# Kernel optimization log

Hardware: AMD Instinct MI355X
Metric: run time of the kernel (lower is better)

The kernel has to match this reference:

```python
import jax, jax.numpy as jnp
import numpy as np

EPS = 1e-5  # torch InstanceNorm2d default eps


def conv1x1(x, w, b):
    # x: [B,C,H,W], w: [O,C], b: [O]
    return jnp.einsum('bchw,oc->bohw', x, w) + b[None, :, None, None]


def conv3x3(x, w, b):
    y = jax.lax.conv_general_dilated(x, w, (1, 1), 'SAME',
                                     dimension_numbers=('NCHW', 'OIHW', 'NCHW'))
    return y + b[None, :, None, None]


def inorm(x):
    # InstanceNorm2d, affine=False, biased variance
    m = jnp.mean(x, axis=(2, 3), keepdims=True)
    v = jnp.var(x, axis=(2, 3), keepdims=True)
    return (x - m) * jax.lax.rsqrt(v + EPS)


def self_attn(x, wq, bq, wk, bk, wv, bv, gamma):
    B, C, H, W = x.shape
    N = H * W
    q = conv1x1(x, wq, bq).reshape(B, -1, N)   # [B,C/8,N]
    k = conv1x1(x, wk, bk).reshape(B, -1, N)   # [B,C/8,N]
    A = jax.nn.softmax(jnp.einsum('bdn,bdm->bnm', q, k), axis=-1)  # [B,N,N]
    v = conv1x1(x, wv, bv).reshape(B, C, N)    # [B,C,N]
    out = jnp.einsum('bcm,bnm->bcn', v, A).reshape(B, C, H, W)
    return gamma * out + x


def setup_inputs() -> dict:
    key = jax.random.key(0)
    B, C, H, W = 2, 256, 64, 64
    C8 = C // 8
    ks = iter(jax.random.split(key, 40))

    def n(shape, scale=0.05):
        return jax.random.normal(next(ks), shape, dtype=jnp.float32) * scale

    inp = {
        'x': jax.random.normal(next(ks), (B, C, H, W), dtype=jnp.float32),
        'y': jax.random.normal(next(ks), (B, C, H, W), dtype=jnp.float32),
    }
    for p in ('sa1', 'sa2', 'top'):
        inp[p + '_wq'] = n((C8, C)); inp[p + '_bq'] = n((C8,))
        inp[p + '_wk'] = n((C8, C)); inp[p + '_bk'] = n((C8,))
        inp[p + '_wv'] = n((C, C));  inp[p + '_bv'] = n((C,))
        inp[p + '_gamma'] = n((1,), 0.1)
    inp['conv1_w'] = n((C, C, 3, 3)); inp['conv1_b'] = n((C,))
    inp['conv2_w'] = n((C, C, 3, 3)); inp['conv2_b'] = n((C,))
    return inp


def reference(x, y,
              sa1_wq, sa1_bq, sa1_wk, sa1_bk, sa1_wv, sa1_bv, sa1_gamma,
              sa2_wq, sa2_bq, sa2_wk, sa2_bk, sa2_wv, sa2_bv, sa2_gamma,
              top_wq, top_bq, top_wk, top_bk, top_wv, top_bv, top_gamma,
              conv1_w, conv1_b, conv2_w, conv2_b):
    out_1 = inorm(self_attn(x, sa1_wq, sa1_bq, sa1_wk, sa1_bk, sa1_wv, sa1_bv, sa1_gamma))
    out_2 = inorm(out_1 + conv3x3(out_1, conv1_w, conv1_b))
    out_3 = inorm(self_attn(y, sa2_wq, sa2_bq, sa2_wk, sa2_bk, sa2_wv, sa2_bv, sa2_gamma))

    B, C, H, W = out_2.shape
    N = H * W
    q = conv1x1(out_2, top_wq, top_bq).reshape(B, -1, N)
    k = conv1x1(out_2, top_wk, top_bk).reshape(B, -1, N)
    A = jax.nn.softmax(jnp.einsum('bdn,bdm->bnm', q, k), axis=-1)
    v = conv1x1(out_3, top_wv, top_bv).reshape(B, C, N)
    out = jnp.einsum('bcm,bnm->bcn', v, A).reshape(B, C, H, W)
    out = top_gamma * out + y
    out = inorm(out)
    out = inorm(out + out_3)
    out_4 = conv3x3(out, conv2_w, conv2_b)
    out = inorm(out + out_4)
    return out
```

## Files before the change

### kernel.cpp

```cpp
#include <hip/hip_runtime.h>
#include <hip/hip_bf16.h>

typedef __hip_bfloat16 bf16;
typedef __attribute__((ext_vector_type(8))) short s8v;
typedef __attribute__((ext_vector_type(4))) short s4v;
typedef __attribute__((ext_vector_type(4))) float f4v;

#define NPIX 4096
#define CDIM 256
#define MN_ELEMS (1 << 20)
#define QKVSTR (320L * NPIX)
#define QKTSTR (64L * NPIX)

#if __has_builtin(__builtin_amdgcn_exp2f)
#define EXP2F(x) __builtin_amdgcn_exp2f(x)
#else
#define EXP2F(x) exp2f(x)
#endif

typedef __attribute__((address_space(1))) const unsigned int g_u32;
typedef __attribute__((address_space(3))) unsigned int l_u32;
__device__ __forceinline__ void glds16(const void* g, void* l) {
  __builtin_amdgcn_global_load_lds((g_u32*)g, (l_u32*)l, 16, 0, 0);
}

__device__ inline s8v ld8(const bf16* p) { return *(const s8v*)p; }
__device__ inline s8v ld8(const float* p) {
  float4 f0 = *(const float4*)p;
  float4 f1 = *(const float4*)(p + 4);
  s8v r; bf16* e = (bf16*)&r;
  e[0] = __float2bfloat16(f0.x); e[1] = __float2bfloat16(f0.y);
  e[2] = __float2bfloat16(f0.z); e[3] = __float2bfloat16(f0.w);
  e[4] = __float2bfloat16(f1.x); e[5] = __float2bfloat16(f1.y);
  e[6] = __float2bfloat16(f1.z); e[7] = __float2bfloat16(f1.w);
  return r;
}

template<int NT>
__global__ __launch_bounds__(256) void fattn_k(
    const bf16* __restrict__ qkt, const bf16* __restrict__ Vg,
    bf16* __restrict__ out)
{
  constexpr int SN = NT / 32;
  __shared__ bf16 k_s[128 * 32];
  __shared__ bf16 v_s[4 * 128 * 32];
  __shared__ bf16 p_s[4 * NT * 32];
  float* sums = (float*)k_s;

  const int tid = threadIdx.x;
  const int z = blockIdx.z;
  const int w = tid >> 6, lane = tid & 63;
  const int l15 = lane & 15, oct = lane >> 4;
  const int wr = w >> 1, wc = w & 1;
  const int n0 = blockIdx.x * NT, c0 = blockIdx.y * 128;
  const bf16* qk = qkt + (long)z * QKTSTR;
  const bf16* Vz = Vg + (long)z * QKVSTR;
  const int srow = lane >> 2, scol = (lane & 3) * 8;

  #pragma unroll
  for (int g = 0; g < NT / 64; ++g)
    glds16(qk + (long)(n0 + g * 64 + (w << 4) + srow) * 64 + scol,
           p_s + g * 2048 + w * 512);
  glds16(qk + (long)((w << 4) + srow) * 64 + 32 + scol, k_s + w * 512);
  glds16(qk + (long)(64 + (w << 4) + srow) * 64 + 32 + scol, k_s + 2048 + w * 512);
  #pragma unroll
  for (int g = 0; g < 8; ++g) {
    const int kk = g & 3, rg = g >> 2;
    glds16(Vz + (long)(c0 + rg * 64 + (w << 4) + srow) * 4096 + kk * 32 + scol,
           v_s + kk * 4096 + rg * 2048 + w * 512);
  }
  __syncthreads();

  s8v qf[SN];
  #pragma unroll
  for (int st = 0; st < SN; ++st)
    qf[st] = *(const s8v*)(p_s + (wr * (NT / 2) + st * 16 + l15) * 32 + oct * 8);
  __syncthreads();

  f4v acc[4][SN];
  #pragma unroll
  for (int i = 0; i < 4; ++i)
    #pragma unroll
    for (int j = 0; j < SN; ++j) acc[i][j] = (f4v){0.f, 0.f, 0.f, 0.f};
  float rs[SN];
  #pragma unroll
  for (int st = 0; st < SN; ++st) rs[st] = 0.f;

  for (int i = 0; i < 32; ++i) {
    s8v kf[4];
    #pragma unroll
    for (int nt = 0; nt < 4; ++nt)
      kf[nt] = *(const s8v*)(k_s + (wc * 64 + nt * 16 + l15) * 32 + oct * 8);
    #pragma unroll
    for (int st = 0; st < SN; ++st) {
      const int n = wr * (NT / 2) + st * 16 + l15;
      const int sw = ((n >> 1) & 3) << 4;
      f4v sa[4];
      __builtin_amdgcn_s_setprio(1);
      #pragma unroll
      for (int nt = 0; nt < 4; ++nt) {
        f4v zz = (f4v){0.f, 0.f, 0.f, 0.f};
        sa[nt] = __builtin_amdgcn_mfma_f32_16x16x32_bf16(kf[nt], qf[st], zz, 0, 0, 0);
      }
      __builtin_amdgcn_s_setprio(0);
      #pragma unroll
      for (int nt = 0; nt < 4; ++nt) {
        const int kk = wc * 2 + (nt >> 1);
        int byte = kk * (NT * 64) + n * 64 + (nt & 1) * 32 + oct * 8;
        byte ^= sw;
        s4v pk; bf16* pe = (bf16*)&pk;
        float rsum = 0.f;
        #pragma unroll
        for (int r = 0; r < 4; ++r) {
          float e = EXP2F(sa[nt][r]);
          rsum += e;
          pe[r] = __float2bfloat16(e);
        }
        rs[st] += rsum;
        *(s4v*)((char*)p_s + byte) = pk;
      }
    }
    __syncthreads();
    #pragma unroll
    for (int kk = 0; kk < 4; ++kk) {
      s8v vf[4], pf[SN];
      #pragma unroll
      for (int st = 0; st < 4; ++st)
        vf[st] = *(const s8v*)(v_s + kk * 4096 + (wr * 64 + st * 16 + l15) * 32 + oct * 8);
      #pragma unroll
      for (int nt = 0; nt < SN; ++nt) {
        const int n = wc * (NT / 2) + nt * 16 + l15;
        int byte = kk * (NT * 64) + n * 64 + oct * 16;
        byte ^= ((n >> 1) & 3) << 4;
        pf[nt] = *(const s8v*)((const char*)p_s + byte);
      }
      __builtin_amdgcn_s_setprio(1);
      #pragma unroll
      for (int st = 0; st < 4; ++st)
        #pragma unroll
        for (int nt = 0; nt < SN; ++nt)
          acc[st][nt] = __builtin_amdgcn_mfma_f32_16x16x32_bf16(vf[st], pf[nt], acc[st][nt], 0, 0, 0);
      __builtin_amdgcn_s_setprio(0);
    }
    __syncthreads();
    if (i < 31) {
      const int m1 = (i + 1) * 128;
      glds16(qk + (long)(m1 + (w << 4) + srow) * 64 + 32 + scol, k_s + w * 512);
      glds16(qk + (long)(m1 + 64 + (w << 4) + srow) * 64 + 32 + scol, k_s + 2048 + w * 512);
      #pragma unroll
      for (int g = 0; g < 8; ++g) {
        const int kk = g & 3, rg = g >> 2;
        glds16(Vz + (long)(c0 + rg * 64 + (w << 4) + srow) * 4096 + m1 + kk * 32 + scol,
               v_s + kk * 4096 + rg * 2048 + w * 512);
      }
      __syncthreads();
    }
  }

  #pragma unroll
  for (int st = 0; st < SN; ++st) {
    rs[st] += __shfl_xor(rs[st], 16);
    rs[st] += __shfl_xor(rs[st], 32);
  }
  if (lane < 16) {
    #pragma unroll
    for (int st = 0; st < SN; ++st)
      sums[wc * NT + wr * (NT / 2) + st * 16 + l15] = rs[st];
  }
  __syncthreads();

  float rinv[SN];
  #pragma unroll
  for (int nt = 0; nt < SN; ++nt) {
    const int n = wc * (NT / 2) + nt * 16 + l15;
    rinv[nt] = 1.f / (sums[n] + sums[NT + n]);
  }
  bf16* op = out + (long)z * ((long)CDIM * NPIX);
  #pragma unroll
  for (int st = 0; st < 4; ++st) {
    const int gc = c0 + wr * 64 + st * 16 + oct * 4;
    #pragma unroll
    for (int nt = 0; nt < SN; ++nt) {
      const int gn = n0 + wc * (NT / 2) + nt * 16 + l15;
      #pragma unroll
      for (int r = 0; r < 4; ++r)
        op[(long)(gc + r) * NPIX + gn] = __float2bfloat16(acc[st][nt][r] * rinv[nt]);
    }
  }
}

__global__ __launch_bounds__(256) void gemm128(
    const bf16* __restrict__ A, const bf16* __restrict__ Bm,
    bf16* __restrict__ Cp, int N, int K, int nchunk, int nsplit,
    long abat, long bbat)
{
  __shared__ bf16 a_s0[128 * 32], a_s1[128 * 32];
  __shared__ bf16 b_s0[128 * 32], b_s1[128 * 32];
  const int tid = threadIdx.x;
  const int z = blockIdx.z;
  const int bb = z / nsplit, ks = z - bb * nsplit;
  A  += bb * abat;
  Bm += bb * bbat;
  const int w = tid >> 6, lane = tid & 63;
  const int l15 = lane & 15, oct = lane >> 4;
  const int wr = w >> 1, wc = w & 1;
  const int m0 = blockIdx.y * 128, n0 = blockIdx.x * 128;
  const int kc0 = ks * nchunk, kc1 = kc0 + nchunk;

  const int srow = lane >> 2, skoff = (lane & 3) * 8;
  const long aRow0 = (long)(m0 + (w << 4) + srow) * K;
  const long aRow1 = (long)(m0 + ((w + 4) << 4) + srow) * K;
  const long bRow0 = (long)(n0 + (w << 4) + srow) * K;
  const long bRow1 = (long)(n0 + ((w + 4) << 4) + srow) * K;
  const int ldsOff0 = (w) * 512, ldsOff1 = (w + 4) * 512;

  f4v acc[4][4];
  #pragma unroll
  for (int i = 0; i < 4; ++i)
    #pragma unroll
    for (int j = 0; j < 4; ++j) acc[i][j] = (f4v){0.f, 0.f, 0.f, 0.f};

  for (int kc = kc0; kc < kc1; ++kc) {
    const int kb0 = kc * 64 + skoff;
    const int kb1 = kb0 + 32;
    glds16(A + aRow0 + kb0, a_s0 + ldsOff0);
    glds16(A + aRow1 + kb0, a_s0 + ldsOff1);
    glds16(A + aRow0 + kb1, a_s1 + ldsOff0);
    glds16(A + aRow1 + kb1, a_s1 + ldsOff1);
    glds16(Bm + bRow0 + kb0, b_s0 + ldsOff0);
    glds16(Bm + bRow1 + kb0, b_s0 + ldsOff1);
    glds16(Bm + bRow0 + kb1, b_s1 + ldsOff0);
    glds16(Bm + bRow1 + kb1, b_s1 + ldsOff1);
    __syncthreads();
    #pragma unroll
    for (int h = 0; h < 2; ++h) {
      const bf16* as = h ? a_s1 : a_s0;
      const bf16* bs = h ? b_s1 : b_s0;
      s8v af[4], bfv[4];
      #pragma unroll
      for (int st = 0; st < 4; ++st)
        af[st] = *(const s8v*)(as + (wr * 64 + st * 16 + l15) * 32 + oct * 8);
      #pragma unroll
      for (int nt = 0; nt < 4; ++nt)
        bfv[nt] = *(const s8v*)(bs + (wc * 64 + nt * 16 + l15) * 32 + oct * 8);
      #pragma unroll
      for (int st = 0; st < 4; ++st)
        #pragma unroll
        for (int nt = 0; nt < 4; ++nt)
          acc[st][nt] = __builtin_amdgcn_mfma_f32_16x16x32_bf16(af[st], bfv[nt], acc[st][nt], 0, 0, 0);
    }
    __syncthreads();
  }

  bf16* Cz = Cp + (long)z * ((long)gridDim.y * 128) * N;
  #pragma unroll
  for (int st = 0; st < 4; ++st) {
    const int gm = m0 + wr * 64 + st * 16 + oct * 4;
    #pragma unroll
    for (int nt = 0; nt < 4; ++nt) {
      const int gn = n0 + wc * 64 + nt * 16 + l15;
      #pragma unroll
      for (int r = 0; r < 4; ++r)
        Cz[(long)(gm + r) * N + gn] = __float2bfloat16(acc[st][nt][r]);
    }
  }
}

template<int QKT, typename TBe>
__global__ __launch_bounds__(256) void proj_k(
    const float* __restrict__ A, const float* __restrict__ A2,
    const TBe* __restrict__ B1, const TBe* __restrict__ B2,
    const float* __restrict__ bias, const float* __restrict__ bias2,
    bf16* __restrict__ Cm, bf16* __restrict__ qkt,
    int M, int N, int K, long bbat, long cbat, int nchunk)
{
  __shared__ bf16 a_s[64][40];
  __shared__ bf16 b_s[64][40];
  const int tid = threadIdx.x;
  const int z = blockIdx.z, stage = z >> 1, bat = z & 1;
  const float* Au = stage ? A2 : A;
  const float* biasu = stage ? bias2 : bias;
  const TBe* Bm = (stage ? B2 : B1) + bat * bbat;
  Cm += z * cbat;
  if (QKT) qkt += z * QKTSTR;
  const int m0 = blockIdx.y * 64, n0 = blockIdx.x * 64;
  const int w = tid >> 6, lane = tid & 63;
  const int l15 = lane & 15, oct = lane >> 4;

  f4v acc[4];
  #pragma unroll
  for (int i = 0; i < 4; ++i) acc[i] = (f4v){0.f, 0.f, 0.f, 0.f};

  const int a_i0 = tid >> 2, a_i1 = (tid & 3) * 8;
  const int b_i0 = tid >> 3, b_i1 = (tid & 7) * 8;

  s8v pa, pb;
  auto ldA = [&](int kc, s8v& d) {
    if (m0 + a_i0 < M) d = ld8(Au + (long)(m0 + a_i0) * K + kc * 32 + a_i1);
    else d = (s8v){0,0,0,0,0,0,0,0};
  };
  auto ldB = [&](int kc, s8v& d) {
    d = ld8(Bm + (long)(kc * 32 + b_i0) * N + n0 + b_i1);
  };

  ldA(0, pa); ldB(0, pb);
  for (int kc = 0; kc < nchunk; ++kc) {
    *(s8v*)&a_s[a_i0][a_i1] = pa;
    {
      const bf16* e = (const bf16*)&pb;
      #pragma unroll
      for (int j = 0; j < 8; ++j) b_s[b_i1 + j][b_i0] = e[j];
    }
    __syncthreads();
    if (kc + 1 < nchunk) { ldA(kc + 1, pa); ldB(kc + 1, pb); }
    s8v af = *(const s8v*)&a_s[w * 16 + l15][oct * 8];
    #pragma unroll
    for (int nt = 0; nt < 4; ++nt) {
      s8v bfr = *(const s8v*)&b_s[nt * 16 + l15][oct * 8];
      acc[nt] = __builtin_amdgcn_mfma_f32_16x16x32_bf16(af, bfr, acc[nt], 0, 0, 0);
    }
    __syncthreads();
  }
  const int gm_base = m0 + w * 16 + oct * 4;
  #pragma unroll
  for (int nt = 0; nt < 4; ++nt) {
    const int gn = n0 + nt * 16 + l15;
    #pragma unroll
    for (int r = 0; r < 4; ++r) {
      int gm = gm_base + r;
      if (gm < M) {
        float vv = acc[nt][r] + biasu[gm];
        if (QKT && gm < 64) {
          float vv2 = (gm < 32) ? vv * 1.44269504f : vv;
          qkt[(long)gn * 64 + gm] = __float2bfloat16(vv2);
        } else {
          Cm[(long)gm * N + gn] = __float2bfloat16(vv);
        }
      }
    }
  }
}

__global__ __launch_bounds__(256) void reduce_bias_k(
    const bf16* __restrict__ part, const float* __restrict__ bias,
    bf16* __restrict__ out, int nsplit)
{
  const int g8 = (blockIdx.x * 256 + threadIdx.x) * 8;
  const int b = g8 >> 20, i = g8 & (MN_ELEMS - 1);
  const bf16* p0 = part + (long)b * nsplit * MN_ELEMS + i;
  float s[8];
  { s8v v = *(const s8v*)p0; const bf16* e = (const bf16*)&v;
    #pragma unroll
    for (int j = 0; j < 8; ++j) s[j] = __bfloat162float(e[j]); }
  for (int p = 1; p < nsplit; ++p) {
    s8v v = *(const s8v*)(p0 + (long)p * MN_ELEMS); const bf16* e = (const bf16*)&v;
    #pragma unroll
    for (int j = 0; j < 8; ++j) s[j] += __bfloat162float(e[j]);
  }
  float bv = bias[i >> 12];
  s8v o; bf16* eo = (bf16*)&o;
  #pragma unroll
  for (int j = 0; j < 8; ++j) eo[j] = __float2bfloat16(s[j] + bv);
  *(s8v*)(out + g8) = o;
}

__global__ __launch_bounds__(256) void cat_k(
    const float* __restrict__ wq, const float* __restrict__ bq,
    const float* __restrict__ wk, const float* __restrict__ bk,
    const float* __restrict__ wv, const float* __restrict__ bv,
    float* __restrict__ wcat, float* __restrict__ bcat, int M)
{
  int idx = blockIdx.x * 256 + threadIdx.x;
  int total = M << 8;
  if (idx < total) {
    int r = idx >> 8, c = idx & 255;
    float v;
    if (r < 32) v = wq[r * 256 + c];
    else if (r < 64) v = wk[(r - 32) * 256 + c];
    else v = wv[(r - 64) * 256 + c];
    wcat[idx] = v;
  } else if (idx < total + M) {
    int r = idx - total;
    bcat[r] = (r < 32) ? bq[r] : (r < 64) ? bk[r - 32] : bv[r - 64];
  }
}

__global__ __launch_bounds__(256) void cvtw2_k(
    const float* __restrict__ w1, const float* __restrict__ w2,
    bf16* __restrict__ o1, bf16* __restrict__ o2)
{
  const float* in = blockIdx.y ? w2 : w1;
  bf16* out = blockIdx.y ? o2 : o1;
  int idx = blockIdx.x * 256 + threadIdx.x;
  int o = idx / 2304, r = idx % 2304;
  int j = r >> 8, c = r & 255;
  out[idx] = __float2bfloat16(in[(o * 256 + c) * 9 + j]);
}

__global__ __launch_bounds__(256) void im2colT2_k(const bf16* __restrict__ x,
                                                  bf16* __restrict__ colT)
{
  __shared__ bf16 lds[3 * 66 * 66];
  const int tid = threadIdx.x;
  const int h = blockIdx.x, c0 = blockIdx.y * 64;
  x    += (long)blockIdx.z * CDIM * NPIX;
  colT += (long)blockIdx.z * 2304L * NPIX;

  if (tid < 192) {
    int row = tid >> 6, c = tid & 63;
    lds[(row * 66 + 0) * 66 + c] = __float2bfloat16(0.f);
    lds[(row * 66 + 65) * 66 + c] = __float2bfloat16(0.f);
  }
  const int w2 = tid & 31, chi = tid >> 5;
  #pragma unroll
  for (int it = 0; it < 24; ++it) {
    int row = it >> 3, cg = it & 7;
    int c = cg * 8 + chi;
    int hh = h + row - 1;
    unsigned int pix = 0;
    if ((unsigned)hh < 64u)
      pix = *(const unsigned int*)(x + (long)(c0 + c) * 4096 + hh * 64 + w2 * 2);
    const bf16* pp = (const bf16*)&pix;
    lds[(row * 66 + (w2 * 2 + 1)) * 66 + c] = pp[0];
    lds[(row * 66 + (w2 * 2 + 2)) * 66 + c] = pp[1];
  }
  __syncthreads();
  const int cg8 = tid & 7, wq = tid >> 3;
  #pragma unroll
  for (int j = 0; j < 9; ++j) {
    const int dy = j / 3, dx = j % 3;
    #pragma unroll
    for (int half = 0; half < 2; ++half) {
      int w = wq + half * 32;
      s8v v = *(const s8v*)&lds[(dy * 66 + (w + dx)) * 66 + cg8 * 8];
      *(s8v*)(colT + (long)(h * 64 + w) * 2304 + j * 256 + c0 + cg8 * 8) = v;
    }
  }
}

__device__ inline void ld16(const bf16* p, float* v) {
  s8v r0 = *(const s8v*)p, r1 = *(const s8v*)(p + 8);
  const bf16* e0 = (const bf16*)&r0; const bf16* e1 = (const bf16*)&r1;
  #pragma unroll
  for (int j = 0; j < 8; ++j) { v[j] = __bfloat162float(e0[j]); v[8 + j] = __bfloat162float(e1[j]); }
}
__device__ inline void ld16(const float* p, float* v) {
  #pragma unroll
  for (int q = 0; q < 4; ++q) {
    float4 f = *(const float4*)(p + q * 4);
    v[q * 4 + 0] = f.x; v[q * 4 + 1] = f.y; v[q * 4 + 2] = f.z; v[q * 4 + 3] = f.w;
  }
}
__device__ inline void st16(bf16* p, const float* v) {
  s8v o0, o1v; bf16* f0 = (bf16*)&o0; bf16* f1 = (bf16*)&o1v;
  #pragma unroll
  for (int j = 0; j < 8; ++j) { f0[j] = __float2bfloat16(v[j]); f1[j] = __float2bfloat16(v[8 + j]); }
  *(s8v*)p = o0; *(s8v*)(p + 8) = o1v;
}
__device__ inline void st16(float* p, const float* v) {
  #pragma unroll
  for (int q = 0; q < 4; ++q) {
    float4 f; f.x = v[q * 4 + 0]; f.y = v[q * 4 + 1]; f.z = v[q * 4 + 2]; f.w = v[q * 4 + 3];
    *(float4*)(p + q * 4) = f;
  }
}

template<typename TAe, typename TBe, typename TOe, int G>
__global__ __launch_bounds__(256) void inorm_k(
    const TAe* __restrict__ a, const TBe* __restrict__ b,
    const float* __restrict__ g, TOe* __restrict__ out)
{
  __shared__ float red[8];
  const int tid = threadIdx.x;
  const long base = (long)blockIdx.x * NPIX + tid * 16;
  float gv = G ? *g : 1.f;
  float va[16], vbv[16], v[16];
  ld16(a + base, va);
  ld16(b + base, vbv);
  #pragma unroll
  for (int j = 0; j < 16; ++j) v[j] = gv * va[j] + vbv[j];
  float sum = 0.f, sq = 0.f;
  #pragma unroll
  for (int j = 0; j < 16; ++j) { sum += v[j]; sq += v[j] * v[j]; }
  #pragma unroll
  for (int s = 32; s; s >>= 1) { sum += __shfl_xor(sum, s); sq += __shfl_xor(sq, s); }
  if ((tid & 63) == 0) { red[tid >> 6] = sum; red[4 + (tid >> 6)] = sq; }
  __syncthreads();
  sum = red[0] + red[1] + red[2] + red[3];
  sq  = red[4] + red[5] + red[6] + red[7];
  float mean = sum * (1.f / NPIX);
  float var  = fmaxf(sq * (1.f / NPIX) - mean * mean, 0.f);
  float rstd = rsqrtf(var + 1e-5f);
  float o[16];
  #pragma unroll
  for (int j = 0; j < 16; ++j) o[j] = (v[j] - mean) * rstd;
  st16(out + base, o);
}

static const long CN = (long)CDIM * NPIX;

static void attn_core(int nb, bf16* qkv, bf16* qkt, bf16* t0, hipStream_t stream)
{
  fattn_k<64><<<dim3(64, 2, nb), dim3(256), 0, stream>>>(qkt, qkv + 64 * NPIX, t0);
}

static void run_conv(const bf16* src, const bf16* wcvt, const float* cb,
                     bf16* colT, bf16* part, bf16* dst, hipStream_t stream)
{
  dim3 TB(256);
  im2colT2_k<<<dim3(64, 4, 2), TB, 0, stream>>>(src, colT);
  gemm128<<<dim3(32, 2, 8), TB, 0, stream>>>(wcvt, colT, part, NPIX, 2304, 9, 4,
                                             0L, 2304L * NPIX);
  reduce_bias_k<<<dim3(1024), TB, 0, stream>>>(part, cb, dst, 4);
}

extern "C" void kernel_launch(void* const* d_in, const int* in_sizes, int n_in,
                              void* d_out, int out_size, void* d_ws, size_t ws_size,
                              hipStream_t stream)
{
  (void)in_sizes; (void)n_in; (void)out_size; (void)ws_size;
  const float* x = (const float*)d_in[0];
  const float* y = (const float*)d_in[1];
  auto W = [&](int i) { return (const float*)d_in[i]; };

  char* wp = (char*)d_ws;
  auto take = [&](size_t nbytes) { char* p = wp; wp += (nbytes + 255) & ~(size_t)255; return p; };
  bf16*  qkv   = (bf16*)take((size_t)4 * QKVSTR * 2);
  bf16*  qkt   = (bf16*)take((size_t)4 * QKTSTR * 2);
  bf16*  t0    = (bf16*)take((size_t)4 * CN * 2);
  bf16*  u1    = (bf16*)take(2 * CN * 2);
  bf16*  u2    = (bf16*)take(2 * CN * 2);
  bf16*  u3    = (bf16*)take(2 * CN * 2);
  bf16*  u4    = (bf16*)take(2 * CN * 2);
  bf16*  colT  = (bf16*)take((size_t)2 * 2304L * NPIX * 2);
  bf16*  wcvt1 = (bf16*)take((size_t)589824 * 2);
  bf16*  wcvt2 = (bf16*)take((size_t)589824 * 2);
  float* wcat1 = (float*)take((size_t)81920 * 4);
  float* bcat1 = (float*)take(320 * 4);
  float* wcat2 = (float*)take((size_t)81920 * 4);
  float* bcat2 = (float*)take(320 * 4);
  float* wqk   = (float*)take((size_t)16384 * 4);
  float* bqk   = (float*)take(64 * 4);
  bf16*  part  = (bf16*)take((size_t)8 * MN_ELEMS * 2);
  bf16*  cvout = qkv;

  dim3 TB(256);

  cat_k<<<dim3(322), TB, 0, stream>>>(W(2), W(3), W(4), W(5), W(6), W(7), wcat1, bcat1, 320);
  cat_k<<<dim3(322), TB, 0, stream>>>(W(9), W(10), W(11), W(12), W(13), W(14), wcat2, bcat2, 320);
  cat_k<<<dim3(65),  TB, 0, stream>>>(W(16), W(17), W(18), W(19), nullptr, nullptr, wqk, bqk, 64);
  cvtw2_k<<<dim3(2304, 2), TB, 0, stream>>>(W(23), W(25), wcvt1, wcvt2);

  proj_k<1,float><<<dim3(64,5,4), TB, 0, stream>>>(
      wcat1, wcat2, x, y, bcat1, bcat2, qkv, qkt, 320, NPIX, 256, CN, QKVSTR, 8);
  attn_core(4, qkv, qkt, t0, stream);

  inorm_k<bf16,float,bf16,1><<<dim3(512), TB, 0, stream>>>(t0, x, W(8), u1);
  inorm_k<bf16,float,bf16,1><<<dim3(512), TB, 0, stream>>>(t0 + 2 * CN, y, W(15), u3);

  run_conv(u1, wcvt1, W(24), colT, part, cvout, stream);
  inorm_k<bf16,bf16,bf16,0><<<dim3(512), TB, 0, stream>>>(u1, cvout, nullptr, u2);

  proj_k<1,bf16><<<dim3(64,1,2), TB, 0, stream>>>(
      wqk, wqk, u2, u2, bqk, bqk, qkv, qkt, 64, NPIX, 256, CN, QKVSTR, 8);
  proj_k<0,bf16><<<dim3(64,4,2), TB, 0, stream>>>(
      W(20), W(20), u3, u3, W(21), W(21), qkv + 64 * NPIX, qkt, 256, NPIX, 256, CN, QKVSTR, 8);
  attn_core(2, qkv, qkt, t0, stream);
  inorm_k<bf16,float,bf16,1><<<dim3(512), TB, 0, stream>>>(t0, y, W(22), u1);
  inorm_k<bf16,bf16,bf16,0><<<dim3(512), TB, 0, stream>>>(u1, u3, nullptr, u4);
  run_conv(u4, wcvt2, W(26), colT, part, cvout, stream);
  inorm_k<bf16,bf16,float,0><<<dim3(512), TB, 0, stream>>>(u4, cvout, nullptr, (float*)d_out);
}
```

Baseline: 396.0 us.

## Load V fragments directly into registers in flash-attention kernel, dropping LDS staging

Removes the V shared-memory buffer and instead has each wave load its own V operand fragments straight from global memory into registers at the start of each key block. The PV MMA is re-partitioned so each wave owns 32 channels across all NT query columns, rather than a 2x2 wave grid. The next K tile prefetch moves ahead of the PV loop, which removes one barrier per iteration. This frees a large block of LDS and cuts synchronisation, but the V global loads are now exposed latency inside the loop, and each wave reads more P fragments from LDS.

```diff
diff --git a/kernel.cpp b/kernel.cpp
--- a/kernel.cpp
+++ b/kernel.cpp
@@ -41,9 +41,9 @@
     const bf16* __restrict__ qkt, const bf16* __restrict__ Vg,
     bf16* __restrict__ out)
 {
-  constexpr int SN = NT / 32;
+  constexpr int SN  = NT / 32;
+  constexpr int NST = NT / 16;
   __shared__ bf16 k_s[128 * 32];
-  __shared__ bf16 v_s[4 * 128 * 32];
   __shared__ bf16 p_s[4 * NT * 32];
   float* sums = (float*)k_s;
 
@@ -57,18 +57,15 @@
   const bf16* Vz = Vg + (long)z * QKVSTR;
   const int srow = lane >> 2, scol = (lane & 3) * 8;
 
+  const bf16* vb0 = Vz + (long)(c0 + w * 32 + l15) * 4096 + oct * 8;
+  const bf16* vb1 = vb0 + 16L * 4096;
+
   #pragma unroll
   for (int g = 0; g < NT / 64; ++g)
     glds16(qk + (long)(n0 + g * 64 + (w << 4) + srow) * 64 + scol,
            p_s + g * 2048 + w * 512);
   glds16(qk + (long)((w << 4) + srow) * 64 + 32 + scol, k_s + w * 512);
   glds16(qk + (long)(64 + (w << 4) + srow) * 64 + 32 + scol, k_s + 2048 + w * 512);
-  #pragma unroll
-  for (int g = 0; g < 8; ++g) {
-    const int kk = g & 3, rg = g >> 2;
-    glds16(Vz + (long)(c0 + rg * 64 + (w << 4) + srow) * 4096 + kk * 32 + scol,
-           v_s + kk * 4096 + rg * 2048 + w * 512);
-  }
   __syncthreads();
 
   s8v qf[SN];
@@ -77,16 +74,22 @@
     qf[st] = *(const s8v*)(p_s + (wr * (NT / 2) + st * 16 + l15) * 32 + oct * 8);
   __syncthreads();
 
-  f4v acc[4][SN];
-  #pragma unroll
-  for (int i = 0; i < 4; ++i)
-    #pragma unroll
-    for (int j = 0; j < SN; ++j) acc[i][j] = (f4v){0.f, 0.f, 0.f, 0.f};
+  f4v acc[2][NST];
+  #pragma unroll
+  for (int i = 0; i < 2; ++i)
+    #pragma unroll
+    for (int j = 0; j < NST; ++j) acc[i][j] = (f4v){0.f, 0.f, 0.f, 0.f};
   float rs[SN];
   #pragma unroll
   for (int st = 0; st < SN; ++st) rs[st] = 0.f;
 
   for (int i = 0; i < 32; ++i) {
+    s8v vreg[2][4];
+    #pragma unroll
+    for (int kk = 0; kk < 4; ++kk) {
+      vreg[0][kk] = *(const s8v*)(vb0 + (long)i * 128 + kk * 32);
+      vreg[1][kk] = *(const s8v*)(vb1 + (long)i * 128 + kk * 32);
+    }
     s8v kf[4];
     #pragma unroll
     for (int nt = 0; nt < 4; ++nt)
@@ -121,40 +124,30 @@
       }
     }
     __syncthreads();
+    if (i < 31) {
+      const int m1 = (i + 1) * 128;
+      glds16(qk + (long)(m1 + (w << 4) + srow) * 64 + 32 + scol, k_s + w * 512);
+      glds16(qk + (long)(m1 + 64 + (w << 4) + srow) * 64 + 32 + scol, k_s + 2048 + w * 512);
+    }
     #pragma unroll
     for (int kk = 0; kk < 4; ++kk) {
-      s8v vf[4], pf[SN];
-      #pragma unroll
-      for (int st = 0; st < 4; ++st)
-        vf[st] = *(const s8v*)(v_s + kk * 4096 + (wr * 64 + st * 16 + l15) * 32 + oct * 8);
-      #pragma unroll
-      for (int nt = 0; nt < SN; ++nt) {
-        const int n = wc * (NT / 2) + nt * 16 + l15;
+      s8v pf[NST];
+      #pragma unroll
+      for (int nt = 0; nt < NST; ++nt) {
+        const int n = nt * 16 + l15;
         int byte = kk * (NT * 64) + n * 64 + oct * 16;
         byte ^= ((n >> 1) & 3) << 4;
         pf[nt] = *(const s8v*)((const char*)p_s + byte);
       }
       __builtin_amdgcn_s_setprio(1);
       #pragma unroll
-      for (int st = 0; st < 4; ++st)
+      for (int st = 0; st < 2; ++st)
         #pragma unroll
-        for (int nt = 0; nt < SN; ++nt)
-          acc[st][nt] = __builtin_amdgcn_mfma_f32_16x16x32_bf16(vf[st], pf[nt], acc[st][nt], 0, 0, 0);
+        for (int nt = 0; nt < NST; ++nt)
+          acc[st][nt] = __builtin_amdgcn_mfma_f32_16x16x32_bf16(vreg[st][kk], pf[nt], acc[st][nt], 0, 0, 0);
       __builtin_amdgcn_s_setprio(0);
     }
     __syncthreads();
-    if (i < 31) {
-      const int m1 = (i + 1) * 128;
-      glds16(qk + (long)(m1 + (w << 4) + srow) * 64 + 32 + scol, k_s + w * 512);
-      glds16(qk + (long)(m1 + 64 + (w << 4) + srow) * 64 + 32 + scol, k_s + 2048 + w * 512);
-      #pragma unroll
-      for (int g = 0; g < 8; ++g) {
-        const int kk = g & 3, rg = g >> 2;
-        glds16(Vz + (long)(c0 + rg * 64 + (w << 4) + srow) * 4096 + m1 + kk * 32 + scol,
-               v_s + kk * 4096 + rg * 2048 + w * 512);
-      }
-      __syncthreads();
-    }
   }
 
   #pragma unroll
@@ -169,19 +162,19 @@
   }
   __syncthreads();
 
-  float rinv[SN];
-  #pragma unroll
-  for (int nt = 0; nt < SN; ++nt) {
-    const int n = wc * (NT / 2) + nt * 16 + l15;
+  float rinv[NST];
+  #pragma unroll
+  for (int nt = 0; nt < NST; ++nt) {
+    const int n = nt * 16 + l15;
     rinv[nt] = 1.f / (sums[n] + sums[NT + n]);
   }
   bf16* op = out + (long)z * ((long)CDIM * NPIX);
   #pragma unroll
-  for (int st = 0; st < 4; ++st) {
-    const int gc = c0 + wr * 64 + st * 16 + oct * 4;
-    #pragma unroll
-    for (int nt = 0; nt < SN; ++nt) {
-      const int gn = n0 + wc * (NT / 2) + nt * 16 + l15;
+  for (int st = 0; st < 2; ++st) {
+    const int gc = c0 + w * 32 + st * 16 + oct * 4;
+    #pragma unroll
+    for (int nt = 0; nt < NST; ++nt) {
+      const int gn = n0 + nt * 16 + l15;
       #pragma unroll
       for (int r = 0; r < 4; ++r)
         op[(long)(gc + r) * NPIX + gn] = __float2bfloat16(acc[st][nt][r] * rinv[nt]);
```

New measurement: 399.2 us. About the same (+0.8%).

## Fuse im2col, split-K GEMM and bias reduce into one implicit-GEMM conv kernel

Applied to the files above, without the earlier changes.

Replaces the three-kernel 3x3 conv path (im2col into a large buffer, split-K GEMM writing bf16 partials, then a reduce-plus-bias pass) with one implicit-GEMM kernel. The new kernel stages a 3-row halo of 64 input channels in LDS, reads bf16 weights straight from global memory, and adds the bias in its epilogue. The aim is to drop the im2col and partial-sum memory traffic and two launches. In exchange the grid shrinks to 256 blocks with no split-K, weight fragments are loaded from global with no LDS reuse, and the loads are not double-buffered, so latency hiding may be weaker.

```diff
diff --git a/kernel.cpp b/kernel.cpp
--- a/kernel.cpp
+++ b/kernel.cpp
@@ -189,80 +189,73 @@
   }
 }
 
-__global__ __launch_bounds__(256) void gemm128(
-    const bf16* __restrict__ A, const bf16* __restrict__ Bm,
-    bf16* __restrict__ Cp, int N, int K, int nchunk, int nsplit,
-    long abat, long bbat)
-{
-  __shared__ bf16 a_s0[128 * 32], a_s1[128 * 32];
-  __shared__ bf16 b_s0[128 * 32], b_s1[128 * 32];
+__global__ __launch_bounds__(512) void conv_k(
+    const bf16* __restrict__ x, const bf16* __restrict__ wcvt,
+    const float* __restrict__ bias, bf16* __restrict__ out)
+{
+  __shared__ bf16 lds[3 * 66 * 66];
   const int tid = threadIdx.x;
-  const int z = blockIdx.z;
-  const int bb = z / nsplit, ks = z - bb * nsplit;
-  A  += bb * abat;
-  Bm += bb * bbat;
+  const int h = blockIdx.x;
+  const int o0 = blockIdx.y * 128;
+  x   += (long)blockIdx.z * CDIM * NPIX;
+  out += (long)blockIdx.z * CDIM * NPIX;
+
   const int w = tid >> 6, lane = tid & 63;
   const int l15 = lane & 15, oct = lane >> 4;
-  const int wr = w >> 1, wc = w & 1;
-  const int m0 = blockIdx.y * 128, n0 = blockIdx.x * 128;
-  const int kc0 = ks * nchunk, kc1 = kc0 + nchunk;
-
-  const int srow = lane >> 2, skoff = (lane & 3) * 8;
-  const long aRow0 = (long)(m0 + (w << 4) + srow) * K;
-  const long aRow1 = (long)(m0 + ((w + 4) << 4) + srow) * K;
-  const long bRow0 = (long)(n0 + (w << 4) + srow) * K;
-  const long bRow1 = (long)(n0 + ((w + 4) << 4) + srow) * K;
-  const int ldsOff0 = (w) * 512, ldsOff1 = (w + 4) * 512;
-
-  f4v acc[4][4];
-  #pragma unroll
-  for (int i = 0; i < 4; ++i)
-    #pragma unroll
-    for (int j = 0; j < 4; ++j) acc[i][j] = (f4v){0.f, 0.f, 0.f, 0.f};
-
-  for (int kc = kc0; kc < kc1; ++kc) {
-    const int kb0 = kc * 64 + skoff;
-    const int kb1 = kb0 + 32;
-    glds16(A + aRow0 + kb0, a_s0 + ldsOff0);
-    glds16(A + aRow1 + kb0, a_s0 + ldsOff1);
-    glds16(A + aRow0 + kb1, a_s1 + ldsOff0);
-    glds16(A + aRow1 + kb1, a_s1 + ldsOff1);
-    glds16(Bm + bRow0 + kb0, b_s0 + ldsOff0);
-    glds16(Bm + bRow1 + kb0, b_s0 + ldsOff1);
-    glds16(Bm + bRow0 + kb1, b_s1 + ldsOff0);
-    glds16(Bm + bRow1 + kb1, b_s1 + ldsOff1);
-    __syncthreads();
-    #pragma unroll
-    for (int h = 0; h < 2; ++h) {
-      const bf16* as = h ? a_s1 : a_s0;
-      const bf16* bs = h ? b_s1 : b_s0;
-      s8v af[4], bfv[4];
-      #pragma unroll
-      for (int st = 0; st < 4; ++st)
-        af[st] = *(const s8v*)(as + (wr * 64 + st * 16 + l15) * 32 + oct * 8);
-      #pragma unroll
-      for (int nt = 0; nt < 4; ++nt)
-        bfv[nt] = *(const s8v*)(bs + (wc * 64 + nt * 16 + l15) * 32 + oct * 8);
-      #pragma unroll
-      for (int st = 0; st < 4; ++st)
+
+  if (tid < 192) {
+    int row = tid >> 6, c = tid & 63;
+    lds[(row * 66 + 0) * 66 + c] = __float2bfloat16(0.f);
+    lds[(row * 66 + 65) * 66 + c] = __float2bfloat16(0.f);
+  }
+
+  f4v acc[4];
+  #pragma unroll
+  for (int nf = 0; nf < 4; ++nf) acc[nf] = (f4v){0.f, 0.f, 0.f, 0.f};
+
+  const int w2 = tid & 31, chi = tid >> 5;
+  const long arow = (long)(o0 + w * 16 + l15) * 2304;
+
+  for (int cg = 0; cg < 4; ++cg) {
+    __syncthreads();
+    #pragma unroll
+    for (int it = 0; it < 12; ++it) {
+      int row = it >> 2, cgi = it & 3;
+      int c = cgi * 16 + chi;
+      int hh = h + row - 1;
+      unsigned int pix = 0;
+      if ((unsigned)hh < 64u)
+        pix = *(const unsigned int*)(x + (long)(cg * 64 + c) * 4096 + hh * 64 + w2 * 2);
+      const bf16* pp = (const bf16*)&pix;
+      lds[(row * 66 + (w2 * 2 + 1)) * 66 + c] = pp[0];
+      lds[(row * 66 + (w2 * 2 + 2)) * 66 + c] = pp[1];
+    }
+    __syncthreads();
+
+    #pragma unroll
+    for (int j = 0; j < 9; ++j) {
+      const int dy = j / 3, dx = j % 3;
+      #pragma unroll
+      for (int kc = 0; kc < 2; ++kc) {
+        s8v af = *(const s8v*)(wcvt + arow + j * 256 + cg * 64 + kc * 32 + oct * 8);
+        s8v bfv[4];
         #pragma unroll
-        for (int nt = 0; nt < 4; ++nt)
-          acc[st][nt] = __builtin_amdgcn_mfma_f32_16x16x32_bf16(af[st], bfv[nt], acc[st][nt], 0, 0, 0);
-    }
-    __syncthreads();
-  }
-
-  bf16* Cz = Cp + (long)z * ((long)gridDim.y * 128) * N;
-  #pragma unroll
-  for (int st = 0; st < 4; ++st) {
-    const int gm = m0 + wr * 64 + st * 16 + oct * 4;
-    #pragma unroll
-    for (int nt = 0; nt < 4; ++nt) {
-      const int gn = n0 + wc * 64 + nt * 16 + l15;
-      #pragma unroll
-      for (int r = 0; r < 4; ++r)
-        Cz[(long)(gm + r) * N + gn] = __float2bfloat16(acc[st][nt][r]);
-    }
+        for (int nf = 0; nf < 4; ++nf)
+          bfv[nf] = *(const s8v*)&lds[(dy * 66 + (nf * 16 + l15 + dx)) * 66 + kc * 32 + oct * 8];
+        #pragma unroll
+        for (int nf = 0; nf < 4; ++nf)
+          acc[nf] = __builtin_amdgcn_mfma_f32_16x16x32_bf16(af, bfv[nf], acc[nf], 0, 0, 0);
+      }
+    }
+  }
+
+  #pragma unroll
+  for (int nf = 0; nf < 4; ++nf) {
+    const int gn = h * 64 + nf * 16 + l15;
+    const int go = o0 + w * 16 + oct * 4;
+    #pragma unroll
+    for (int r = 0; r < 4; ++r)
+      out[(long)(go + r) * NPIX + gn] = __float2bfloat16(acc[nf][r] + bias[go + r]);
   }
 }
 
@@ -341,29 +334,6 @@
   }
 }
 
-__global__ __launch_bounds__(256) void reduce_bias_k(
-    const bf16* __restrict__ part, const float* __restrict__ bias,
-    bf16* __restrict__ out, int nsplit)
-{
-  const int g8 = (blockIdx.x * 256 + threadIdx.x) * 8;
-  const int b = g8 >> 20, i = g8 & (MN_ELEMS - 1);
-  const bf16* p0 = part + (long)b * nsplit * MN_ELEMS + i;
-  float s[8];
-  { s8v v = *(const s8v*)p0; const bf16* e = (const bf16*)&v;
-    #pragma unroll
-    for (int j = 0; j < 8; ++j) s[j] = __bfloat162float(e[j]); }
-  for (int p = 1; p < nsplit; ++p) {
-    s8v v = *(const s8v*)(p0 + (long)p * MN_ELEMS); const bf16* e = (const bf16*)&v;
-    #pragma unroll
-    for (int j = 0; j < 8; ++j) s[j] += __bfloat162float(e[j]);
-  }
-  float bv = bias[i >> 12];
-  s8v o; bf16* eo = (bf16*)&o;
-  #pragma unroll
-  for (int j = 0; j < 8; ++j) eo[j] = __float2bfloat16(s[j] + bv);
-  *(s8v*)(out + g8) = o;
-}
-
 __global__ __launch_bounds__(256) void cat_k(
     const float* __restrict__ wq, const float* __restrict__ bq,
     const float* __restrict__ wk, const float* __restrict__ bk,
@@ -397,47 +367,6 @@
   out[idx] = __float2bfloat16(in[(o * 256 + c) * 9 + j]);
 }
 
-__global__ __launch_bounds__(256) void im2colT2_k(const bf16* __restrict__ x,
-                                                  bf16* __restrict__ colT)
-{
-  __shared__ bf16 lds[3 * 66 * 66];
-  const int tid = threadIdx.x;
-  const int h = blockIdx.x, c0 = blockIdx.y * 64;
-  x    += (long)blockIdx.z * CDIM * NPIX;
-  colT += (long)blockIdx.z * 2304L * NPIX;
-
-  if (tid < 192) {
-    int row = tid >> 6, c = tid & 63;
-    lds[(row * 66 + 0) * 66 + c] = __float2bfloat16(0.f);
-    lds[(row * 66 + 65) * 66 + c] = __float2bfloat16(0.f);
-  }
-  const int w2 = tid & 31, chi = tid >> 5;
-  #pragma unroll
-  for (int it = 0; it < 24; ++it) {
-    int row = it >> 3, cg = it & 7;
-    int c = cg * 8 + chi;
-    int hh = h + row - 1;
-    unsigned int pix = 0;
-    if ((unsigned)hh < 64u)
-      pix = *(const unsigned int*)(x + (long)(c0 + c) * 4096 + hh * 64 + w2 * 2);
-    const bf16* pp = (const bf16*)&pix;
-    lds[(row * 66 + (w2 * 2 + 1)) * 66 + c] = pp[0];
-    lds[(row * 66 + (w2 * 2 + 2)) * 66 + c] = pp[1];
-  }
-  __syncthreads();
-  const int cg8 = tid & 7, wq = tid >> 3;
-  #pragma unroll
-  for (int j = 0; j < 9; ++j) {
-    const int dy = j / 3, dx = j % 3;
-    #pragma unroll
-    for (int half = 0; half < 2; ++half) {
-      int w = wq + half * 32;
-      s8v v = *(const s8v*)&lds[(dy * 66 + (w + dx)) * 66 + cg8 * 8];
-      *(s8v*)(colT + (long)(h * 64 + w) * 2304 + j * 256 + c0 + cg8 * 8) = v;
-    }
-  }
-}
-
 __device__ inline void ld16(const bf16* p, float* v) {
   s8v r0 = *(const s8v*)p, r1 = *(const s8v*)(p + 8);
   const bf16* e0 = (const bf16*)&r0; const bf16* e1 = (const bf16*)&r1;
@@ -505,13 +434,9 @@
 }
 
 static void run_conv(const bf16* src, const bf16* wcvt, const float* cb,
-                     bf16* colT, bf16* part, bf16* dst, hipStream_t stream)
-{
-  dim3 TB(256);
-  im2colT2_k<<<dim3(64, 4, 2), TB, 0, stream>>>(src, colT);
-  gemm128<<<dim3(32, 2, 8), TB, 0, stream>>>(wcvt, colT, part, NPIX, 2304, 9, 4,
-                                             0L, 2304L * NPIX);
-  reduce_bias_k<<<dim3(1024), TB, 0, stream>>>(part, cb, dst, 4);
+                     bf16* dst, hipStream_t stream)
+{
+  conv_k<<<dim3(64, 2, 2), dim3(512), 0, stream>>>(src, wcvt, cb, dst);
 }
 
 extern "C" void kernel_launch(void* const* d_in, const int* in_sizes, int n_in,
@@ -532,7 +457,6 @@
   bf16*  u2    = (bf16*)take(2 * CN * 2);
   bf16*  u3    = (bf16*)take(2 * CN * 2);
   bf16*  u4    = (bf16*)take(2 * CN * 2);
-  bf16*  colT  = (bf16*)take((size_t)2 * 2304L * NPIX * 2);
   bf16*  wcvt1 = (bf16*)take((size_t)589824 * 2);
   bf16*  wcvt2 = (bf16*)take((size_t)589824 * 2);
   float* wcat1 = (float*)take((size_t)81920 * 4);
@@ -541,7 +465,6 @@
   float* bcat2 = (float*)take(320 * 4);
   float* wqk   = (float*)take((size_t)16384 * 4);
   float* bqk   = (float*)take(64 * 4);
-  bf16*  part  = (bf16*)take((size_t)8 * MN_ELEMS * 2);
   bf16*  cvout = qkv;
 
   dim3 TB(256);
@@ -558,7 +481,7 @@
   inorm_k<bf16,float,bf16,1><<<dim3(512), TB, 0, stream>>>(t0, x, W(8), u1);
   inorm_k<bf16,float,bf16,1><<<dim3(512), TB, 0, stream>>>(t0 + 2 * CN, y, W(15), u3);
 
-  run_conv(u1, wcvt1, W(24), colT, part, cvout, stream);
+  run_conv(u1, wcvt1, W(24), cvout, stream);
   inorm_k<bf16,bf16,bf16,0><<<dim3(512), TB, 0, stream>>>(u1, cvout, nullptr, u2);
 
   proj_k<1,bf16><<<dim3(64,1,2), TB, 0, stream>>>(
@@ -568,6 +491,6 @@
   attn_core(2, qkv, qkt, t0, stream);
   inorm_k<bf16,float,bf16,1><<<dim3(512), TB, 0, stream>>>(t0, y, W(22), u1);
   inorm_k<bf16,bf16,bf16,0><<<dim3(512), TB, 0, stream>>>(u1, u3, nullptr, u4);
-  run_conv(u4, wcvt2, W(26), colT, part, cvout, stream);
+  run_conv(u4, wcvt2, W(26), cvout, stream);
   inorm_k<bf16,bf16,float,0><<<dim3(512), TB, 0, stream>>>(u4, cvout, nullptr, (float*)d_out);
 }
```

After: 381.4 us. -3.7%, faster.
